# Optimization experiments

Measured on AMD Instinct MI355X. Metric: run time of the kernel, lower is better.

Reference implementation:

```python
import jax, jax.numpy as jnp
import numpy as np

B = 65536
NREQ = 2097152
NVEH = 1048576
NPAS = 2097152
E = 4194304


def _xavier(key, fi, fo):
    gain = 5.0 / 3.0  # tanh gain
    std = gain * np.sqrt(2.0 / (fi + fo))
    return jax.random.normal(key, (fi, fo), dtype=jnp.float32) * std


def scatter_mean(x, idx, num_segments):
    s = jax.ops.segment_sum(x, idx, num_segments=num_segments)
    c = jax.ops.segment_sum(jnp.ones((x.shape[0], 1), x.dtype), idx, num_segments=num_segments)
    return s / jnp.maximum(c, 1.0)


def setup_inputs() -> dict:
    key = jax.random.key(0)
    ks = jax.random.split(key, 16)
    inp = {
        "requests_x": jax.random.normal(ks[0], (NREQ, 10), dtype=jnp.float32),
        "requests_x_batch": jnp.sort(jax.random.randint(ks[1], (NREQ,), 0, B)),
        "vehicles_x": jax.random.normal(ks[2], (NVEH, 8), dtype=jnp.float32),
        "vehicles_x_batch": jnp.sort(jax.random.randint(ks[3], (NVEH,), 0, B)),
        "passengers_x": jax.random.normal(ks[4], (NPAS, 10), dtype=jnp.float32),
        "veh2pas_receiver_edge_index": jax.random.randint(ks[5], (E,), 0, NPAS),
        "veh2pas_sender_edge_index": jax.random.randint(ks[6], (E,), 0, NVEH),
        "req2veh_receiver_start_index": jax.random.randint(ks[7], (B,), 0, NVEH),
        "W_req": _xavier(ks[8], 10, 16), "b_req": jnp.zeros((16,), jnp.float32),
        "W_veh": _xavier(ks[9], 8, 16), "b_veh": jnp.zeros((16,), jnp.float32),
        "W_pas": _xavier(ks[10], 10, 16), "b_pas": jnp.zeros((16,), jnp.float32),
        "W1": _xavier(ks[11], 64, 64), "b1": jnp.zeros((64,), jnp.float32),
        "W2": _xavier(ks[12], 64, 64), "b2": jnp.zeros((64,), jnp.float32),
        "W3": _xavier(ks[13], 64, 1), "b3": jnp.zeros((1,), jnp.float32),
    }
    return inp


def reference(requests_x, requests_x_batch, vehicles_x, vehicles_x_batch, passengers_x,
              veh2pas_receiver_edge_index, veh2pas_sender_edge_index,
              req2veh_receiver_start_index,
              W_req, b_req, W_veh, b_veh, W_pas, b_pas, W1, b1, W2, b2, W3, b3):
    # per-node-type small MLPs
    req_feat = jnp.tanh(requests_x @ W_req + b_req)            # [NREQ,16]
    req_mean = scatter_mean(req_feat, requests_x_batch, B)      # [B,16]
    veh_feat = jnp.tanh(vehicles_x @ W_veh + b_veh)             # [NVEH,16]
    pas_feat = jnp.tanh(passengers_x @ W_pas + b_pas)           # [NPAS,16]
    # gather passengers along edges, mean-pool onto vehicles
    pas_mean = scatter_mean(pas_feat[veh2pas_receiver_edge_index],
                            veh2pas_sender_edge_index, NVEH)    # [NVEH,16]
    ego_feat = jnp.concatenate([veh_feat, pas_mean], axis=-1)[req2veh_receiver_start_index]  # [B,32]
    veh_mean = scatter_mean(veh_feat, vehicles_x_batch, B)      # [B,16]
    action_feat = jnp.concatenate([req_mean, ego_feat, veh_mean], axis=-1)  # [B,64]
    h = jnp.tanh(action_feat @ W1 + b1)
    h = jnp.tanh(h @ W2 + b2)
    return h @ W3 + b3                                          # [B,1]
```

## Files before the change

### kernel.cpp

```cpp
#include <hip/hip_runtime.h>
#include <cstddef>
#include <cstdint>

#define TPB 256
#define BATCH 65536
#define NREQ 2097152
#define NVEH 1048576
#define NEDGE 4194304
#define CAP 32
#define RSENT 0xFFFFu

__device__ __forceinline__ float fast_tanh(float x) {
    float e = __expf(2.0f * x);
    return 1.0f - 2.0f / (e + 1.0f);
}
__device__ __forceinline__ float4 tanh4(float4 v) {
    return make_float4(fast_tanh(v.x), fast_tanh(v.y), fast_tanh(v.z), fast_tanh(v.w));
}

__global__ __launch_bounds__(TPB) void k_bounds(
    const int* __restrict__ req_batch, const int* __restrict__ veh_batch,
    const int* __restrict__ req2veh,
    int* __restrict__ seg_req, int* __restrict__ seg_veh,
    unsigned* __restrict__ markbits, unsigned short* __restrict__ rank16,
    int* __restrict__ cnt)
{
    int t = blockIdx.x * TPB + threadIdx.x;
    int i0 = t * 4;
    {
        int4 c = *reinterpret_cast<const int4*>(req_batch + i0);
        int prev = (i0 == 0) ? -1 : req_batch[i0 - 1];
        int vals[4] = {c.x, c.y, c.z, c.w};
        #pragma unroll
        for (int u = 0; u < 4; ++u) {
            for (int b = prev + 1; b <= vals[u]; ++b) seg_req[b] = i0 + u;
            prev = vals[u];
        }
        if (i0 + 4 == NREQ)
            for (int b = prev + 1; b <= BATCH; ++b) seg_req[b] = NREQ;
    }
    if (i0 < NVEH) {
        int4 c = *reinterpret_cast<const int4*>(veh_batch + i0);
        int prev = (i0 == 0) ? -1 : veh_batch[i0 - 1];
        int vals[4] = {c.x, c.y, c.z, c.w};
        #pragma unroll
        for (int u = 0; u < 4; ++u) {
            for (int b = prev + 1; b <= vals[u]; ++b) seg_veh[b] = i0 + u;
            prev = vals[u];
        }
        if (i0 + 4 == NVEH)
            for (int b = prev + 1; b <= BATCH; ++b) seg_veh[b] = NVEH;
    }
    if (i0 < BATCH) {
        int4 vv = *reinterpret_cast<const int4*>(req2veh + i0);
        int vs[4] = {vv.x, vv.y, vv.z, vv.w};
        #pragma unroll
        for (int u = 0; u < 4; ++u) {
            int v = vs[u];
            unsigned bit = 1u << (v & 31);
            unsigned old = atomicOr(&markbits[v >> 5], bit);
            if (!(old & bit))
                rank16[v] = (unsigned short)atomicAdd(cnt, 1);
        }
    }
}

template<int F>
__device__ __forceinline__ void mlp_acc(
    const float* xr, const float4* wq, float4 bq, float4& s)
{
    float4 a = bq;
    #pragma unroll
    for (int i = 0; i < F; ++i) {
        a.x = fmaf(xr[i], wq[i].x, a.x);
        a.y = fmaf(xr[i], wq[i].y, a.y);
        a.z = fmaf(xr[i], wq[i].z, a.z);
        a.w = fmaf(xr[i], wq[i].w, a.w);
    }
    float4 t = tanh4(a);
    s.x += t.x; s.y += t.y; s.z += t.z; s.w += t.w;
}

template<int F>
__device__ __forceinline__ void seg_mean_reg(
    const float* __restrict__ x, const int* __restrict__ seg,
    const float* __restrict__ W, const float* __restrict__ bias,
    float* __restrict__ mean_out, int b, int q)
{
    float4 wq[F];
    #pragma unroll
    for (int i = 0; i < F; ++i)
        wq[i] = *reinterpret_cast<const float4*>(&W[i*16 + q*4]);
    float4 bq = reinterpret_cast<const float4*>(bias)[q];

    int lo = seg[b];
    int hi = seg[b + 1];
    float4 s = make_float4(0.f, 0.f, 0.f, 0.f);

    if constexpr (F == 10) {
        int r = lo;
        if ((r & 1) && r < hi) {
            const float2* p = reinterpret_cast<const float2*>(x + (size_t)r * 10);
            float xr[10];
            #pragma unroll
            for (int i = 0; i < 5; ++i) { float2 t = p[i]; xr[2*i] = t.x; xr[2*i+1] = t.y; }
            mlp_acc<10>(xr, wq, bq, s);
            ++r;
        }
        for (; r + 2 <= hi; r += 2) {
            const float4* p = reinterpret_cast<const float4*>(x + (size_t)r * 10);
            float4 v0 = p[0], v1 = p[1], v2 = p[2], v3 = p[3], v4 = p[4];
            float xr0[10] = {v0.x,v0.y,v0.z,v0.w, v1.x,v1.y,v1.z,v1.w, v2.x,v2.y};
            float xr1[10] = {v2.z,v2.w, v3.x,v3.y,v3.z,v3.w, v4.x,v4.y,v4.z,v4.w};
            mlp_acc<10>(xr0, wq, bq, s);
            mlp_acc<10>(xr1, wq, bq, s);
        }
        if (r < hi) {
            const float2* p = reinterpret_cast<const float2*>(x + (size_t)r * 10);
            float xr[10];
            #pragma unroll
            for (int i = 0; i < 5; ++i) { float2 t = p[i]; xr[2*i] = t.x; xr[2*i+1] = t.y; }
            mlp_acc<10>(xr, wq, bq, s);
        }
    } else {
        int r = lo;
        for (; r + 2 <= hi; r += 2) {
            const float4* p = reinterpret_cast<const float4*>(x + (size_t)r * 8);
            float4 v0 = p[0], v1 = p[1], v2 = p[2], v3 = p[3];
            float xr0[8] = {v0.x,v0.y,v0.z,v0.w, v1.x,v1.y,v1.z,v1.w};
            float xr1[8] = {v2.x,v2.y,v2.z,v2.w, v3.x,v3.y,v3.z,v3.w};
            mlp_acc<8>(xr0, wq, bq, s);
            mlp_acc<8>(xr1, wq, bq, s);
        }
        if (r < hi) {
            const float4* p = reinterpret_cast<const float4*>(x + (size_t)r * 8);
            float4 v0 = p[0], v1 = p[1];
            float xr0[8] = {v0.x,v0.y,v0.z,v0.w, v1.x,v1.y,v1.z,v1.w};
            mlp_acc<8>(xr0, wq, bq, s);
        }
    }
    float inv = 1.0f / fmaxf((float)(hi - lo), 1.0f);
    float4 o = make_float4(s.x*inv, s.y*inv, s.z*inv, s.w*inv);
    reinterpret_cast<float4*>(mean_out)[(size_t)b*4 + q] = o;
}

#define NB_MID 6144

__global__ __launch_bounds__(TPB, 2) void k_mid(
    const float* __restrict__ requests_x, const int* __restrict__ seg_req,
    const float* __restrict__ vehicles_x, const int* __restrict__ seg_veh,
    const float* __restrict__ W_req, const float* __restrict__ b_req,
    const float* __restrict__ W_veh, const float* __restrict__ b_veh,
    float* __restrict__ req_mean, float* __restrict__ veh_mean,
    const int* __restrict__ send, const int* __restrict__ recv,
    const unsigned short* __restrict__ rank16,
    int* __restrict__ deg, int* __restrict__ bucket)
{
    int blk = blockIdx.x, tid = threadIdx.x;
    if (blk % 3 == 0) {
        int p1 = blk / 3;
        if (p1 < 1024) {
            int t = p1 * TPB + tid;
            seg_mean_reg<10>(requests_x, seg_req, W_req, b_req, req_mean, t >> 2, t & 3);
        } else {
            int t = (p1 - 1024) * TPB + tid;
            seg_mean_reg<8>(vehicles_x, seg_veh, W_veh, b_veh, veh_mean, t >> 2, t & 3);
        }
    } else {
        int eid = blk - blk / 3 - 1;
        int e4 = eid * TPB + tid;
        int4 sv = reinterpret_cast<const int4*>(send)[e4];
        int vv[4] = {sv.x, sv.y, sv.z, sv.w};
        #pragma unroll
        for (int u = 0; u < 4; ++u) {
            unsigned r = rank16[vv[u]];
            if (r != RSENT) {
                int slot = atomicAdd(&deg[r], 1);
                if (slot < CAP) bucket[(size_t)r * CAP + slot] = recv[e4 * 4 + u];
            }
        }
    }
}

__global__ __launch_bounds__(TPB, 3) void k_final(
    const float* __restrict__ req_mean, const float* __restrict__ veh_mean,
    const unsigned short* __restrict__ rank16, const int* __restrict__ deg,
    const int* __restrict__ bucket, const float* __restrict__ pas_x,
    const float* __restrict__ vehicles_x, const int* __restrict__ req2veh,
    const float* __restrict__ W_veh, const float* __restrict__ b_veh,
    const float* __restrict__ W_pas, const float* __restrict__ b_pas,
    const float* __restrict__ W1, const float* __restrict__ b1,
    const float* __restrict__ W2, const float* __restrict__ b2,
    const float* __restrict__ W3, const float* __restrict__ b3,
    float* __restrict__ out)
{
    __shared__ __align__(16) float sW1[4096];
    __shared__ __align__(16) float sW2[4096];
    __shared__ float sW3[64];
    __shared__ float sb1[64];
    __shared__ float sb2[64];

    int tid = threadIdx.x;
    {
        const float4* s1 = reinterpret_cast<const float4*>(W1);
        const float4* s2 = reinterpret_cast<const float4*>(W2);
        float4* d1 = reinterpret_cast<float4*>(sW1);
        float4* d2 = reinterpret_cast<float4*>(sW2);
        for (int i = tid; i < 1024; i += TPB) { d1[i] = s1[i]; d2[i] = s2[i]; }
        if (tid < 64) { sW3[tid] = W3[tid]; sb1[tid] = b1[tid]; sb2[tid] = b2[tid]; }
    }
    __syncthreads();

    int q = tid & 3;
    int b = blockIdx.x * (TPB / 4) + (tid >> 2);
    int lane = tid & 63;
    int lbase = lane & ~3;

    float a[64];
    {
        const float4* rs = reinterpret_cast<const float4*>(req_mean) + (size_t)b*4;
        const float4* vs = reinterpret_cast<const float4*>(veh_mean) + (size_t)b*4;
        #pragma unroll
        for (int j4 = 0; j4 < 4; ++j4) {
            float4 t = rs[j4];
            a[4*j4+0]=t.x; a[4*j4+1]=t.y; a[4*j4+2]=t.z; a[4*j4+3]=t.w;
            float4 u = vs[j4];
            a[48+4*j4+0]=u.x; a[48+4*j4+1]=u.y; a[48+4*j4+2]=u.z; a[48+4*j4+3]=u.w;
        }
    }
    int v = req2veh[b];

    float4 fv;
    {
        float4 wv[8];
        #pragma unroll
        for (int i = 0; i < 8; ++i)
            wv[i] = *reinterpret_cast<const float4*>(&W_veh[i*16 + q*4]);
        float4 bv = reinterpret_cast<const float4*>(b_veh)[q];
        const float4* vp = reinterpret_cast<const float4*>(vehicles_x + (size_t)v*8);
        float4 t0 = vp[0], t1 = vp[1];
        float vx[8] = {t0.x,t0.y,t0.z,t0.w,t1.x,t1.y,t1.z,t1.w};
        float4 acc = bv;
        #pragma unroll
        for (int i = 0; i < 8; ++i) {
            acc.x = fmaf(vx[i], wv[i].x, acc.x); acc.y = fmaf(vx[i], wv[i].y, acc.y);
            acc.z = fmaf(vx[i], wv[i].z, acc.z); acc.w = fmaf(vx[i], wv[i].w, acc.w);
        }
        fv = tanh4(acc);
    }

    float4 fp;
    {
        float4 wp[10];
        #pragma unroll
        for (int i = 0; i < 10; ++i)
            wp[i] = *reinterpret_cast<const float4*>(&W_pas[i*16 + q*4]);
        float4 bp = reinterpret_cast<const float4*>(b_pas)[q];
        int rk = rank16[v];
        int d = deg[rk];
        int n = min(d, CAP);
        const int4* bk4 = reinterpret_cast<const int4*>(bucket + (size_t)rk * CAP);
        float4 ps = make_float4(0.f, 0.f, 0.f, 0.f);
        for (int c = 0; c * 4 < n; ++c) {
            int4 idx = bk4[c];
            int pv[4] = {idx.x, idx.y, idx.z, idx.w};
            int m = n - c * 4;
            float px[4][10];
            #pragma unroll
            for (int u = 0; u < 4; ++u) {
                if (u < m) {
                    const float2* pp = reinterpret_cast<const float2*>(pas_x + (size_t)pv[u] * 10);
                    #pragma unroll
                    for (int i = 0; i < 5; ++i) {
                        float2 t = pp[i]; px[u][2*i] = t.x; px[u][2*i+1] = t.y;
                    }
                }
            }
            #pragma unroll
            for (int u = 0; u < 4; ++u) {
                if (u < m) {
                    float4 acc = bp;
                    #pragma unroll
                    for (int i = 0; i < 10; ++i) {
                        acc.x = fmaf(px[u][i], wp[i].x, acc.x);
                        acc.y = fmaf(px[u][i], wp[i].y, acc.y);
                        acc.z = fmaf(px[u][i], wp[i].z, acc.z);
                        acc.w = fmaf(px[u][i], wp[i].w, acc.w);
                    }
                    float4 t = tanh4(acc);
                    ps.x += t.x; ps.y += t.y; ps.z += t.z; ps.w += t.w;
                }
            }
        }
        float inv = 1.0f / fmaxf((float)d, 1.0f);
        fp = make_float4(ps.x*inv, ps.y*inv, ps.z*inv, ps.w*inv);
    }

    #pragma unroll
    for (int src = 0; src < 4; ++src) {
        a[16+4*src+0] = __shfl(fv.x, lbase+src);
        a[16+4*src+1] = __shfl(fv.y, lbase+src);
        a[16+4*src+2] = __shfl(fv.z, lbase+src);
        a[16+4*src+3] = __shfl(fv.w, lbase+src);
        a[32+4*src+0] = __shfl(fp.x, lbase+src);
        a[32+4*src+1] = __shfl(fp.y, lbase+src);
        a[32+4*src+2] = __shfl(fp.z, lbase+src);
        a[32+4*src+3] = __shfl(fp.w, lbase+src);
    }

    const float4* W1v = reinterpret_cast<const float4*>(sW1);
    const float4* W2v = reinterpret_cast<const float4*>(sW2);

    float hq[16];
    {
        float4 acc[4];
        #pragma unroll
        for (int jj = 0; jj < 4; ++jj)
            acc[jj] = *reinterpret_cast<const float4*>(&sb1[q*16 + jj*4]);
        #pragma unroll
        for (int k = 0; k < 64; ++k) {
            float ak = a[k];
            #pragma unroll
            for (int jj = 0; jj < 4; ++jj) {
                float4 w = W1v[k*16 + q*4 + jj];
                acc[jj].x = fmaf(ak, w.x, acc[jj].x); acc[jj].y = fmaf(ak, w.y, acc[jj].y);
                acc[jj].z = fmaf(ak, w.z, acc[jj].z); acc[jj].w = fmaf(ak, w.w, acc[jj].w);
            }
        }
        #pragma unroll
        for (int jj = 0; jj < 4; ++jj) {
            float4 t = tanh4(acc[jj]);
            hq[4*jj+0]=t.x; hq[4*jj+1]=t.y; hq[4*jj+2]=t.z; hq[4*jj+3]=t.w;
        }
    }
    #pragma unroll
    for (int src = 0; src < 4; ++src)
        #pragma unroll
        for (int jj = 0; jj < 16; ++jj)
            a[src*16 + jj] = __shfl(hq[jj], lbase + src);

    float o;
    {
        float4 acc[4];
        #pragma unroll
        for (int jj = 0; jj < 4; ++jj)
            acc[jj] = *reinterpret_cast<const float4*>(&sb2[q*16 + jj*4]);
        #pragma unroll
        for (int k = 0; k < 64; ++k) {
            float ak = a[k];
            #pragma unroll
            for (int jj = 0; jj < 4; ++jj) {
                float4 w = W2v[k*16 + q*4 + jj];
                acc[jj].x = fmaf(ak, w.x, acc[jj].x); acc[jj].y = fmaf(ak, w.y, acc[jj].y);
                acc[jj].z = fmaf(ak, w.z, acc[jj].z); acc[jj].w = fmaf(ak, w.w, acc[jj].w);
            }
        }
        o = 0.0f;
        #pragma unroll
        for (int jj = 0; jj < 4; ++jj) {
            float4 t = tanh4(acc[jj]);
            o = fmaf(t.x, sW3[q*16+4*jj+0], o);
            o = fmaf(t.y, sW3[q*16+4*jj+1], o);
            o = fmaf(t.z, sW3[q*16+4*jj+2], o);
            o = fmaf(t.w, sW3[q*16+4*jj+3], o);
        }
    }
    o += __shfl_xor(o, 1);
    o += __shfl_xor(o, 2);
    if (q == 0) out[b] = o + b3[0];
}

extern "C" void kernel_launch(void* const* d_in, const int* in_sizes, int n_in,
                              void* d_out, int out_size, void* d_ws, size_t ws_size,
                              hipStream_t stream) {
    const float* requests_x = (const float*)d_in[0];
    const int*   req_batch  = (const int*)d_in[1];
    const float* vehicles_x = (const float*)d_in[2];
    const int*   veh_batch  = (const int*)d_in[3];
    const float* pas_x      = (const float*)d_in[4];
    const int*   recv       = (const int*)d_in[5];
    const int*   send       = (const int*)d_in[6];
    const int*   req2veh    = (const int*)d_in[7];
    const float* W_req = (const float*)d_in[8];
    const float* b_req = (const float*)d_in[9];
    const float* W_veh = (const float*)d_in[10];
    const float* b_veh = (const float*)d_in[11];
    const float* W_pas = (const float*)d_in[12];
    const float* b_pas = (const float*)d_in[13];
    const float* W1 = (const float*)d_in[14];
    const float* b1 = (const float*)d_in[15];
    const float* W2 = (const float*)d_in[16];
    const float* b2 = (const float*)d_in[17];
    const float* W3 = (const float*)d_in[18];
    const float* b3 = (const float*)d_in[19];
    float* out = (float*)d_out;

    char* ws = (char*)d_ws;
    float*          req_mean = (float*)         (ws + 0);
    float*          veh_mean = (float*)         (ws + (4u<<20));
    int*            seg_req  = (int*)           (ws + (8u<<20));
    int*            seg_veh  = (int*)           (ws + (9u<<20));
    unsigned*       markbits = (unsigned*)      (ws + (10u<<20));
    int*            deg      = (int*)           (ws + (10u<<20) + (128u<<10));
    int*            cnt      = (int*)           (ws + (10u<<20) + (384u<<10));
    unsigned short* rank16   = (unsigned short*)(ws + (11u<<20));
    int*            bucket   = (int*)           (ws + (13u<<20));

    hipMemsetAsync(markbits, 0, (388u<<10), stream);
    hipMemsetAsync(rank16, 0xFF, NVEH * sizeof(unsigned short), stream);

    k_bounds<<<NREQ/4/TPB, TPB, 0, stream>>>(
        req_batch, veh_batch, req2veh, seg_req, seg_veh, markbits, rank16, cnt);

    k_mid<<<NB_MID, TPB, 0, stream>>>(
        requests_x, seg_req, vehicles_x, seg_veh,
        W_req, b_req, W_veh, b_veh, req_mean, veh_mean,
        send, recv, rank16, deg, bucket);

    k_final<<<BATCH*4/TPB, TPB, 0, stream>>>(
        req_mean, veh_mean, rank16, deg, bucket, pas_x,
        vehicles_x, req2veh, W_veh, b_veh, W_pas, b_pas,
        W1, b1, W2, b2, W3, b3, out);
}
```

Baseline: 160.3 us.

## Double-buffer segment-mean row loads and widen edge-bucket work per thread

The segment-mean loop now loads groups of four rows into two float4 register buffers and computes on one while the next group loads, so more memory requests are in flight per thread. Edge processing handles eight edges per thread and issues all rank16 gathers before the atomics, and the block layout changes from interleaved to contiguous ranges with fewer edge blocks. This raises register pressure from the two buffers, which may reduce occupancy, and segments shorter than eight rows still take the scalar path.

```diff
diff --git a/kernel.cpp b/kernel.cpp
--- a/kernel.cpp
+++ b/kernel.cpp
@@ -66,9 +66,55 @@
 }
 
 template<int F>
-__device__ __forceinline__ void mlp_acc(
-    const float* xr, const float4* wq, float4 bq, float4& s)
-{
+__device__ __forceinline__ float gete(const float4* buf, int idx) {
+    float4 v = buf[idx >> 2];
+    return (idx & 3) == 0 ? v.x : (idx & 3) == 1 ? v.y : (idx & 3) == 2 ? v.z : v.w;
+}
+
+template<int F>
+__device__ __forceinline__ void comp4(
+    const float4* buf, const float4* wq, float4 bq, float4& s)
+{
+    #pragma unroll
+    for (int u = 0; u < 4; ++u) {
+        float4 a = bq;
+        #pragma unroll
+        for (int i = 0; i < F; ++i) {
+            float xv = gete<F>(buf, u * F + i);
+            a.x = fmaf(xv, wq[i].x, a.x);
+            a.y = fmaf(xv, wq[i].y, a.y);
+            a.z = fmaf(xv, wq[i].z, a.z);
+            a.w = fmaf(xv, wq[i].w, a.w);
+        }
+        float4 t = tanh4(a);
+        s.x += t.x; s.y += t.y; s.z += t.z; s.w += t.w;
+    }
+}
+
+template<int F>
+__device__ __forceinline__ void ldgrp(const float* __restrict__ x, int r, float4* buf) {
+    const float4* p;
+    if constexpr (F == 10) p = reinterpret_cast<const float4*>(x) + (size_t)(r >> 1) * 5;
+    else                   p = reinterpret_cast<const float4*>(x) + (size_t)r * 2;
+    #pragma unroll
+    for (int i = 0; i < F; ++i) buf[i] = p[i];
+}
+
+template<int F>
+__device__ __forceinline__ void one_row(
+    const float* __restrict__ x, int r, const float4* wq, float4 bq, float4& s)
+{
+    float xr[F];
+    if constexpr (F == 10) {
+        const float2* p = reinterpret_cast<const float2*>(x + (size_t)r * 10);
+        #pragma unroll
+        for (int i = 0; i < 5; ++i) { float2 t = p[i]; xr[2*i] = t.x; xr[2*i+1] = t.y; }
+    } else {
+        const float4* p = reinterpret_cast<const float4*>(x + (size_t)r * 8);
+        float4 a = p[0], b = p[1];
+        xr[0]=a.x; xr[1]=a.y; xr[2]=a.z; xr[3]=a.w;
+        xr[4]=b.x; xr[5]=b.y; xr[6]=b.z; xr[7]=b.w;
+    }
     float4 a = bq;
     #pragma unroll
     for (int i = 0; i < F; ++i) {
@@ -97,54 +143,41 @@
     int hi = seg[b + 1];
     float4 s = make_float4(0.f, 0.f, 0.f, 0.f);
 
-    if constexpr (F == 10) {
-        int r = lo;
-        if ((r & 1) && r < hi) {
-            const float2* p = reinterpret_cast<const float2*>(x + (size_t)r * 10);
-            float xr[10];
-            #pragma unroll
-            for (int i = 0; i < 5; ++i) { float2 t = p[i]; xr[2*i] = t.x; xr[2*i+1] = t.y; }
-            mlp_acc<10>(xr, wq, bq, s);
-            ++r;
-        }
-        for (; r + 2 <= hi; r += 2) {
-            const float4* p = reinterpret_cast<const float4*>(x + (size_t)r * 10);
-            float4 v0 = p[0], v1 = p[1], v2 = p[2], v3 = p[3], v4 = p[4];
-            float xr0[10] = {v0.x,v0.y,v0.z,v0.w, v1.x,v1.y,v1.z,v1.w, v2.x,v2.y};
-            float xr1[10] = {v2.z,v2.w, v3.x,v3.y,v3.z,v3.w, v4.x,v4.y,v4.z,v4.w};
-            mlp_acc<10>(xr0, wq, bq, s);
-            mlp_acc<10>(xr1, wq, bq, s);
-        }
-        if (r < hi) {
-            const float2* p = reinterpret_cast<const float2*>(x + (size_t)r * 10);
-            float xr[10];
-            #pragma unroll
-            for (int i = 0; i < 5; ++i) { float2 t = p[i]; xr[2*i] = t.x; xr[2*i+1] = t.y; }
-            mlp_acc<10>(xr, wq, bq, s);
-        }
-    } else {
-        int r = lo;
-        for (; r + 2 <= hi; r += 2) {
-            const float4* p = reinterpret_cast<const float4*>(x + (size_t)r * 8);
-            float4 v0 = p[0], v1 = p[1], v2 = p[2], v3 = p[3];
-            float xr0[8] = {v0.x,v0.y,v0.z,v0.w, v1.x,v1.y,v1.z,v1.w};
-            float xr1[8] = {v2.x,v2.y,v2.z,v2.w, v3.x,v3.y,v3.z,v3.w};
-            mlp_acc<8>(xr0, wq, bq, s);
-            mlp_acc<8>(xr1, wq, bq, s);
-        }
-        if (r < hi) {
-            const float4* p = reinterpret_cast<const float4*>(x + (size_t)r * 8);
-            float4 v0 = p[0], v1 = p[1];
-            float xr0[8] = {v0.x,v0.y,v0.z,v0.w, v1.x,v1.y,v1.z,v1.w};
-            mlp_acc<8>(xr0, wq, bq, s);
-        }
-    }
+    int r = lo;
+    if ((r & 1) && r < hi) { one_row<F>(x, r, wq, bq, s); ++r; }
+
+    int n8 = (hi - r) >> 3;
+    if (n8 > 0) {
+        float4 bufA[F], bufB[F];
+        ldgrp<F>(x, r, bufA);
+        ldgrp<F>(x, r + 4, bufB);
+        for (int sg = 1; sg < n8; ++sg) {
+            int rn = r + sg * 8;
+            comp4<F>(bufA, wq, bq, s);
+            ldgrp<F>(x, rn, bufA);
+            comp4<F>(bufB, wq, bq, s);
+            ldgrp<F>(x, rn + 4, bufB);
+        }
+        comp4<F>(bufA, wq, bq, s);
+        comp4<F>(bufB, wq, bq, s);
+        r += n8 * 8;
+    }
+    if (hi - r >= 4) {
+        float4 bufA[F];
+        ldgrp<F>(x, r, bufA);
+        comp4<F>(bufA, wq, bq, s);
+        r += 4;
+    }
+    for (; r < hi; ++r) one_row<F>(x, r, wq, bq, s);
+
     float inv = 1.0f / fmaxf((float)(hi - lo), 1.0f);
     float4 o = make_float4(s.x*inv, s.y*inv, s.z*inv, s.w*inv);
     reinterpret_cast<float4*>(mean_out)[(size_t)b*4 + q] = o;
 }
 
-#define NB_MID 6144
+#define NB_P1   2048
+#define NB_EDGE (NEDGE / (TPB * 8))
+#define NB_MID  (NB_P1 + NB_EDGE)
 
 __global__ __launch_bounds__(TPB, 2) void k_mid(
     const float* __restrict__ requests_x, const int* __restrict__ seg_req,
@@ -157,26 +190,26 @@
     int* __restrict__ deg, int* __restrict__ bucket)
 {
     int blk = blockIdx.x, tid = threadIdx.x;
-    if (blk % 3 == 0) {
-        int p1 = blk / 3;
-        if (p1 < 1024) {
-            int t = p1 * TPB + tid;
-            seg_mean_reg<10>(requests_x, seg_req, W_req, b_req, req_mean, t >> 2, t & 3);
-        } else {
-            int t = (p1 - 1024) * TPB + tid;
-            seg_mean_reg<8>(vehicles_x, seg_veh, W_veh, b_veh, veh_mean, t >> 2, t & 3);
-        }
+    if (blk < 1024) {
+        int t = blk * TPB + tid;
+        seg_mean_reg<10>(requests_x, seg_req, W_req, b_req, req_mean, t >> 2, t & 3);
+    } else if (blk < NB_P1) {
+        int t = (blk - 1024) * TPB + tid;
+        seg_mean_reg<8>(vehicles_x, seg_veh, W_veh, b_veh, veh_mean, t >> 2, t & 3);
     } else {
-        int eid = blk - blk / 3 - 1;
-        int e4 = eid * TPB + tid;
-        int4 sv = reinterpret_cast<const int4*>(send)[e4];
-        int vv[4] = {sv.x, sv.y, sv.z, sv.w};
-        #pragma unroll
-        for (int u = 0; u < 4; ++u) {
-            unsigned r = rank16[vv[u]];
-            if (r != RSENT) {
-                int slot = atomicAdd(&deg[r], 1);
-                if (slot < CAP) bucket[(size_t)r * CAP + slot] = recv[e4 * 4 + u];
+        int e8 = (blk - NB_P1) * TPB + tid;
+        const int4* s4 = reinterpret_cast<const int4*>(send);
+        int4 a0 = s4[(size_t)e8 * 2];
+        int4 a1 = s4[(size_t)e8 * 2 + 1];
+        int vv[8] = {a0.x, a0.y, a0.z, a0.w, a1.x, a1.y, a1.z, a1.w};
+        unsigned rr[8];
+        #pragma unroll
+        for (int u = 0; u < 8; ++u) rr[u] = rank16[vv[u]];
+        #pragma unroll
+        for (int u = 0; u < 8; ++u) {
+            if (rr[u] != RSENT) {
+                int slot = atomicAdd(&deg[rr[u]], 1);
+                if (slot < CAP) bucket[(size_t)rr[u] * CAP + slot] = recv[(size_t)e8 * 8 + u];
             }
         }
     }
```

After: 173.9 us. +8.5%, slower.

## Split segment-mean work across 8 threads per batch and batch rank gathers

Applied to the files above, without the earlier changes.

The segment-mean MLP now gives each batch 8 threads that each own 2 output columns instead of 4 threads owning 4. This doubles parallelism and cuts registers per thread, allowing 4 blocks per SM and a 1:1 interleave of segment blocks with edge-bucketing blocks. The edge bucketing loads all four rank16 values before doing the atomics, so the dependent loads overlap. In exchange, each input row is loaded redundantly by 8 threads instead of 4, and the row loads lose the paired float4 vector path.

```diff
diff --git a/kernel.cpp b/kernel.cpp
--- a/kernel.cpp
+++ b/kernel.cpp
@@ -66,87 +66,71 @@
 }
 
 template<int F>
-__device__ __forceinline__ void mlp_acc(
-    const float* xr, const float4* wq, float4 bq, float4& s)
+__device__ __forceinline__ void row_fma2(
+    const float* xr, const float2* wq, float2 bq, float2& s)
 {
-    float4 a = bq;
+    float ax = bq.x, ay = bq.y;
     #pragma unroll
     for (int i = 0; i < F; ++i) {
-        a.x = fmaf(xr[i], wq[i].x, a.x);
-        a.y = fmaf(xr[i], wq[i].y, a.y);
-        a.z = fmaf(xr[i], wq[i].z, a.z);
-        a.w = fmaf(xr[i], wq[i].w, a.w);
-    }
-    float4 t = tanh4(a);
-    s.x += t.x; s.y += t.y; s.z += t.z; s.w += t.w;
+        ax = fmaf(xr[i], wq[i].x, ax);
+        ay = fmaf(xr[i], wq[i].y, ay);
+    }
+    s.x += fast_tanh(ax);
+    s.y += fast_tanh(ay);
 }
 
 template<int F>
-__device__ __forceinline__ void seg_mean_reg(
+__device__ __forceinline__ void load_row2(const float* __restrict__ x, int r, float* xr) {
+    if constexpr (F == 10) {
+        const float2* p = reinterpret_cast<const float2*>(x + (size_t)r * 10);
+        #pragma unroll
+        for (int i = 0; i < 5; ++i) { float2 t = p[i]; xr[2*i] = t.x; xr[2*i+1] = t.y; }
+    } else {
+        const float4* p = reinterpret_cast<const float4*>(x + (size_t)r * 8);
+        float4 a = p[0], b = p[1];
+        xr[0]=a.x; xr[1]=a.y; xr[2]=a.z; xr[3]=a.w;
+        xr[4]=b.x; xr[5]=b.y; xr[6]=b.z; xr[7]=b.w;
+    }
+}
+
+template<int F>
+__device__ __forceinline__ void seg_mean8(
     const float* __restrict__ x, const int* __restrict__ seg,
     const float* __restrict__ W, const float* __restrict__ bias,
     float* __restrict__ mean_out, int b, int q)
 {
-    float4 wq[F];
+    float2 wq[F];
     #pragma unroll
     for (int i = 0; i < F; ++i)
-        wq[i] = *reinterpret_cast<const float4*>(&W[i*16 + q*4]);
-    float4 bq = reinterpret_cast<const float4*>(bias)[q];
+        wq[i] = *reinterpret_cast<const float2*>(&W[i*16 + q*2]);
+    float2 bq = reinterpret_cast<const float2*>(bias)[q];
 
     int lo = seg[b];
     int hi = seg[b + 1];
-    float4 s = make_float4(0.f, 0.f, 0.f, 0.f);
-
-    if constexpr (F == 10) {
-        int r = lo;
-        if ((r & 1) && r < hi) {
-            const float2* p = reinterpret_cast<const float2*>(x + (size_t)r * 10);
-            float xr[10];
-            #pragma unroll
-            for (int i = 0; i < 5; ++i) { float2 t = p[i]; xr[2*i] = t.x; xr[2*i+1] = t.y; }
-            mlp_acc<10>(xr, wq, bq, s);
-            ++r;
-        }
-        for (; r + 2 <= hi; r += 2) {
-            const float4* p = reinterpret_cast<const float4*>(x + (size_t)r * 10);
-            float4 v0 = p[0], v1 = p[1], v2 = p[2], v3 = p[3], v4 = p[4];
-            float xr0[10] = {v0.x,v0.y,v0.z,v0.w, v1.x,v1.y,v1.z,v1.w, v2.x,v2.y};
-            float xr1[10] = {v2.z,v2.w, v3.x,v3.y,v3.z,v3.w, v4.x,v4.y,v4.z,v4.w};
-            mlp_acc<10>(xr0, wq, bq, s);
-            mlp_acc<10>(xr1, wq, bq, s);
-        }
-        if (r < hi) {
-            const float2* p = reinterpret_cast<const float2*>(x + (size_t)r * 10);
-            float xr[10];
-            #pragma unroll
-            for (int i = 0; i < 5; ++i) { float2 t = p[i]; xr[2*i] = t.x; xr[2*i+1] = t.y; }
-            mlp_acc<10>(xr, wq, bq, s);
-        }
-    } else {
-        int r = lo;
-        for (; r + 2 <= hi; r += 2) {
-            const float4* p = reinterpret_cast<const float4*>(x + (size_t)r * 8);
-            float4 v0 = p[0], v1 = p[1], v2 = p[2], v3 = p[3];
-            float xr0[8] = {v0.x,v0.y,v0.z,v0.w, v1.x,v1.y,v1.z,v1.w};
-            float xr1[8] = {v2.x,v2.y,v2.z,v2.w, v3.x,v3.y,v3.z,v3.w};
-            mlp_acc<8>(xr0, wq, bq, s);
-            mlp_acc<8>(xr1, wq, bq, s);
-        }
-        if (r < hi) {
-            const float4* p = reinterpret_cast<const float4*>(x + (size_t)r * 8);
-            float4 v0 = p[0], v1 = p[1];
-            float xr0[8] = {v0.x,v0.y,v0.z,v0.w, v1.x,v1.y,v1.z,v1.w};
-            mlp_acc<8>(xr0, wq, bq, s);
-        }
-    }
+    float2 s = make_float2(0.f, 0.f);
+
+    int r = lo;
+    for (; r + 2 <= hi; r += 2) {
+        float xr0[F], xr1[F];
+        load_row2<F>(x, r, xr0);
+        load_row2<F>(x, r + 1, xr1);
+        row_fma2<F>(xr0, wq, bq, s);
+        row_fma2<F>(xr1, wq, bq, s);
+    }
+    if (r < hi) {
+        float xr0[F];
+        load_row2<F>(x, r, xr0);
+        row_fma2<F>(xr0, wq, bq, s);
+    }
+
     float inv = 1.0f / fmaxf((float)(hi - lo), 1.0f);
-    float4 o = make_float4(s.x*inv, s.y*inv, s.z*inv, s.w*inv);
-    reinterpret_cast<float4*>(mean_out)[(size_t)b*4 + q] = o;
-}
-
-#define NB_MID 6144
-
-__global__ __launch_bounds__(TPB, 2) void k_mid(
+    float2 o = make_float2(s.x * inv, s.y * inv);
+    reinterpret_cast<float2*>(mean_out)[(size_t)b * 8 + q] = o;
+}
+
+#define NB_MID 8192
+
+__global__ __launch_bounds__(TPB, 4) void k_mid(
     const float* __restrict__ requests_x, const int* __restrict__ seg_req,
     const float* __restrict__ vehicles_x, const int* __restrict__ seg_veh,
     const float* __restrict__ W_req, const float* __restrict__ b_req,
@@ -157,26 +141,28 @@
     int* __restrict__ deg, int* __restrict__ bucket)
 {
     int blk = blockIdx.x, tid = threadIdx.x;
-    if (blk % 3 == 0) {
-        int p1 = blk / 3;
-        if (p1 < 1024) {
+    if ((blk & 1) == 0) {
+        int p1 = blk >> 1;
+        if (p1 < 2048) {
             int t = p1 * TPB + tid;
-            seg_mean_reg<10>(requests_x, seg_req, W_req, b_req, req_mean, t >> 2, t & 3);
+            seg_mean8<10>(requests_x, seg_req, W_req, b_req, req_mean, t >> 3, t & 7);
         } else {
-            int t = (p1 - 1024) * TPB + tid;
-            seg_mean_reg<8>(vehicles_x, seg_veh, W_veh, b_veh, veh_mean, t >> 2, t & 3);
+            int t = (p1 - 2048) * TPB + tid;
+            seg_mean8<8>(vehicles_x, seg_veh, W_veh, b_veh, veh_mean, t >> 3, t & 7);
         }
     } else {
-        int eid = blk - blk / 3 - 1;
+        int eid = blk >> 1;
         int e4 = eid * TPB + tid;
         int4 sv = reinterpret_cast<const int4*>(send)[e4];
         int vv[4] = {sv.x, sv.y, sv.z, sv.w};
+        unsigned rr[4];
+        #pragma unroll
+        for (int u = 0; u < 4; ++u) rr[u] = rank16[vv[u]];
         #pragma unroll
         for (int u = 0; u < 4; ++u) {
-            unsigned r = rank16[vv[u]];
-            if (r != RSENT) {
-                int slot = atomicAdd(&deg[r], 1);
-                if (slot < CAP) bucket[(size_t)r * CAP + slot] = recv[e4 * 4 + u];
+            if (rr[u] != RSENT) {
+                int slot = atomicAdd(&deg[rr[u]], 1);
+                if (slot < CAP) bucket[(size_t)rr[u] * CAP + slot] = recv[e4 * 4 + u];
             }
         }
     }
```

Measured after the change: 185.5 us. 1.16x slower.

## Process four segments per thread team in segment-mean and shrink mean blocks

Applied to the files above, without the earlier changes.

Each 4-lane team now handles four consecutive batch segments at once, interleaving row loads for all four so more independent memory requests are in flight per thread. This cuts the number of segment-mean blocks by four, and the block interleave in k_mid changes from 1-of-3 to 1-of-9 to match, which reduces NB_MID. The cost is more per-thread work and registers, plus divergence when the four segments have different lengths, because out-of-range rows are still loaded (clamped) and then masked.

```diff
diff --git a/kernel.cpp b/kernel.cpp
--- a/kernel.cpp
+++ b/kernel.cpp
@@ -66,6 +66,20 @@
 }
 
 template<int F>
+__device__ __forceinline__ void load_row_p(const float* __restrict__ x, int r, float* xr) {
+    if constexpr (F == 10) {
+        const float2* p = reinterpret_cast<const float2*>(x + (size_t)r * 10);
+        #pragma unroll
+        for (int i = 0; i < 5; ++i) { float2 t = p[i]; xr[2*i] = t.x; xr[2*i+1] = t.y; }
+    } else {
+        const float4* p = reinterpret_cast<const float4*>(x + (size_t)r * 8);
+        float4 a = p[0], b = p[1];
+        xr[0]=a.x; xr[1]=a.y; xr[2]=a.z; xr[3]=a.w;
+        xr[4]=b.x; xr[5]=b.y; xr[6]=b.z; xr[7]=b.w;
+    }
+}
+
+template<int F>
 __device__ __forceinline__ void mlp_acc(
     const float* xr, const float4* wq, float4 bq, float4& s)
 {
@@ -82,10 +96,10 @@
 }
 
 template<int F>
-__device__ __forceinline__ void seg_mean_reg(
+__device__ __forceinline__ void seg_mean4(
     const float* __restrict__ x, const int* __restrict__ seg,
     const float* __restrict__ W, const float* __restrict__ bias,
-    float* __restrict__ mean_out, int b, int q)
+    float* __restrict__ mean_out, int team, int q, int nrows)
 {
     float4 wq[F];
     #pragma unroll
@@ -93,58 +107,43 @@
         wq[i] = *reinterpret_cast<const float4*>(&W[i*16 + q*4]);
     float4 bq = reinterpret_cast<const float4*>(bias)[q];
 
-    int lo = seg[b];
-    int hi = seg[b + 1];
-    float4 s = make_float4(0.f, 0.f, 0.f, 0.f);
-
-    if constexpr (F == 10) {
-        int r = lo;
-        if ((r & 1) && r < hi) {
-            const float2* p = reinterpret_cast<const float2*>(x + (size_t)r * 10);
-            float xr[10];
-            #pragma unroll
-            for (int i = 0; i < 5; ++i) { float2 t = p[i]; xr[2*i] = t.x; xr[2*i+1] = t.y; }
-            mlp_acc<10>(xr, wq, bq, s);
-            ++r;
-        }
-        for (; r + 2 <= hi; r += 2) {
-            const float4* p = reinterpret_cast<const float4*>(x + (size_t)r * 10);
-            float4 v0 = p[0], v1 = p[1], v2 = p[2], v3 = p[3], v4 = p[4];
-            float xr0[10] = {v0.x,v0.y,v0.z,v0.w, v1.x,v1.y,v1.z,v1.w, v2.x,v2.y};
-            float xr1[10] = {v2.z,v2.w, v3.x,v3.y,v3.z,v3.w, v4.x,v4.y,v4.z,v4.w};
-            mlp_acc<10>(xr0, wq, bq, s);
-            mlp_acc<10>(xr1, wq, bq, s);
-        }
-        if (r < hi) {
-            const float2* p = reinterpret_cast<const float2*>(x + (size_t)r * 10);
-            float xr[10];
-            #pragma unroll
-            for (int i = 0; i < 5; ++i) { float2 t = p[i]; xr[2*i] = t.x; xr[2*i+1] = t.y; }
-            mlp_acc<10>(xr, wq, bq, s);
-        }
-    } else {
-        int r = lo;
-        for (; r + 2 <= hi; r += 2) {
-            const float4* p = reinterpret_cast<const float4*>(x + (size_t)r * 8);
-            float4 v0 = p[0], v1 = p[1], v2 = p[2], v3 = p[3];
-            float xr0[8] = {v0.x,v0.y,v0.z,v0.w, v1.x,v1.y,v1.z,v1.w};
-            float xr1[8] = {v2.x,v2.y,v2.z,v2.w, v3.x,v3.y,v3.z,v3.w};
-            mlp_acc<8>(xr0, wq, bq, s);
-            mlp_acc<8>(xr1, wq, bq, s);
-        }
-        if (r < hi) {
-            const float4* p = reinterpret_cast<const float4*>(x + (size_t)r * 8);
-            float4 v0 = p[0], v1 = p[1];
-            float xr0[8] = {v0.x,v0.y,v0.z,v0.w, v1.x,v1.y,v1.z,v1.w};
-            mlp_acc<8>(xr0, wq, bq, s);
-        }
-    }
-    float inv = 1.0f / fmaxf((float)(hi - lo), 1.0f);
-    float4 o = make_float4(s.x*inv, s.y*inv, s.z*inv, s.w*inv);
-    reinterpret_cast<float4*>(mean_out)[(size_t)b*4 + q] = o;
-}
-
-#define NB_MID 6144
+    int base = team * 4;
+    int bnd[5];
+    #pragma unroll
+    for (int k = 0; k < 5; ++k) bnd[k] = seg[base + k];
+    int r[4], hi[4], cnt[4];
+    #pragma unroll
+    for (int k = 0; k < 4; ++k) {
+        r[k] = bnd[k]; hi[k] = bnd[k+1]; cnt[k] = hi[k] - r[k];
+    }
+    float4 acc[4];
+    #pragma unroll
+    for (int k = 0; k < 4; ++k) acc[k] = make_float4(0.f, 0.f, 0.f, 0.f);
+
+    while ((r[0] < hi[0]) | (r[1] < hi[1]) | (r[2] < hi[2]) | (r[3] < hi[3])) {
+        float xr[4][F];
+        #pragma unroll
+        for (int k = 0; k < 4; ++k) {
+            int ra = min(r[k], nrows - 1);
+            load_row_p<F>(x, ra, xr[k]);
+        }
+        #pragma unroll
+        for (int k = 0; k < 4; ++k) {
+            if (r[k] < hi[k]) {
+                mlp_acc<F>(xr[k], wq, bq, acc[k]);
+                ++r[k];
+            }
+        }
+    }
+    #pragma unroll
+    for (int k = 0; k < 4; ++k) {
+        float inv = 1.0f / fmaxf((float)cnt[k], 1.0f);
+        float4 o = make_float4(acc[k].x*inv, acc[k].y*inv, acc[k].z*inv, acc[k].w*inv);
+        reinterpret_cast<float4*>(mean_out)[(size_t)(base + k) * 4 + q] = o;
+    }
+}
+
+#define NB_MID 4608
 
 __global__ __launch_bounds__(TPB, 2) void k_mid(
     const float* __restrict__ requests_x, const int* __restrict__ seg_req,
@@ -157,17 +156,19 @@
     int* __restrict__ deg, int* __restrict__ bucket)
 {
     int blk = blockIdx.x, tid = threadIdx.x;
-    if (blk % 3 == 0) {
-        int p1 = blk / 3;
-        if (p1 < 1024) {
+    if (blk % 9 == 0) {
+        int p1 = blk / 9;
+        if (p1 < 256) {
             int t = p1 * TPB + tid;
-            seg_mean_reg<10>(requests_x, seg_req, W_req, b_req, req_mean, t >> 2, t & 3);
+            seg_mean4<10>(requests_x, seg_req, W_req, b_req, req_mean,
+                          t >> 2, t & 3, NREQ);
         } else {
-            int t = (p1 - 1024) * TPB + tid;
-            seg_mean_reg<8>(vehicles_x, seg_veh, W_veh, b_veh, veh_mean, t >> 2, t & 3);
+            int t = (p1 - 256) * TPB + tid;
+            seg_mean4<8>(vehicles_x, seg_veh, W_veh, b_veh, veh_mean,
+                         t >> 2, t & 3, NVEH);
         }
     } else {
-        int eid = blk - blk / 3 - 1;
+        int eid = blk - blk / 9 - 1;
         int e4 = eid * TPB + tid;
         int4 sv = reinterpret_cast<const int4*>(send)[e4];
         int vv[4] = {sv.x, sv.y, sv.z, sv.w};
```

New measurement: 218.4 us. 1.36x slower.
